# Optimization experiments

Measured on AMD Instinct MI355X. Metric: run time of the kernel, lower is better.

The kernel has to match this reference:

```python
import jax, jax.numpy as jnp
import numpy as np

H = 64
NG = 100000   # gene nodes
ND = 30000    # disease nodes
NE = 1500000  # gda edges (gene -> disease)
NL = 500000   # supervision (label) edges


def setup_inputs() -> dict:
    key = jax.random.key(0)
    ks = jax.random.split(key, 20)
    s = 0.1
    inp = {
        "gene_emb":    jax.random.normal(ks[0], (NG, H), jnp.float32) * s,
        "disease_emb": jax.random.normal(ks[1], (ND, H), jnp.float32) * s,
    }
    wnames = ["w1_gd_l", "w1_gd_r", "w1_dg_l", "w1_dg_r",
              "w2_gd_l", "w2_gd_r", "w2_dg_l", "w2_dg_r"]
    for i, n in enumerate(wnames):
        inp[n] = jax.random.normal(ks[2 + i], (H, H), jnp.float32) * s
    for i, n in enumerate(["b1_gd", "b1_dg", "b2_gd", "b2_dg"]):
        inp[n] = jax.random.normal(ks[10 + i], (H,), jnp.float32) * 0.01
    inp["edge_src"]  = jax.random.randint(ks[14], (NE,), 0, NG)
    inp["edge_dst"]  = jax.random.randint(ks[15], (NE,), 0, ND)
    inp["label_src"] = jax.random.randint(ks[16], (NL,), 0, NG)
    inp["label_dst"] = jax.random.randint(ks[17], (NL,), 0, ND)
    return inp


def _sage(x_src, x_dst, src, dst, n_dst, wl, wr, b):
    # SAGEConv (mean aggr): lin_l(mean_{j in N(i)} x_j) + lin_r(x_i) + b
    msum = jax.ops.segment_sum(x_src[src], dst, num_segments=n_dst)
    cnt = jax.ops.segment_sum(jnp.ones((src.shape[0], 1), x_src.dtype), dst,
                              num_segments=n_dst)
    mean = msum / jnp.maximum(cnt, 1.0)
    return mean @ wl + x_dst @ wr + b


def reference(gene_emb, disease_emb,
              w1_gd_l, w1_gd_r, b1_gd, w1_dg_l, w1_dg_r, b1_dg,
              w2_gd_l, w2_gd_r, b2_gd, w2_dg_l, w2_dg_r, b2_dg,
              edge_src, edge_dst, label_src, label_dst):
    # layer 1 (hetero: gene->disease via gda, disease->gene via rev_gda)
    h_d = jax.nn.relu(_sage(gene_emb, disease_emb, edge_src, edge_dst, ND,
                            w1_gd_l, w1_gd_r, b1_gd))
    h_g = jax.nn.relu(_sage(disease_emb, gene_emb, edge_dst, edge_src, NG,
                            w1_dg_l, w1_dg_r, b1_dg))
    # layer 2 (no activation)
    h_d2 = _sage(h_g, h_d, edge_src, edge_dst, ND, w2_gd_l, w2_gd_r, b2_gd)
    h_g2 = _sage(h_d, h_g, edge_dst, edge_src, NG, w2_dg_l, w2_dg_r, b2_dg)
    # classifier: dot product over label edges
    return jnp.sum(h_g2[label_src] * h_d2[label_dst], axis=-1)
```

## Files before the change

### kernel.cpp

```cpp
#include <hip/hip_runtime.h>
#include <hip/hip_bf16.h>

#define H 64
#define SCAN_CHUNK 512
#define NB1 512

typedef unsigned short u16;
typedef unsigned int u32;
typedef __attribute__((ext_vector_type(8))) __bf16 bf16x8;
typedef __attribute__((ext_vector_type(4))) float f32x4;

__device__ __forceinline__ float bflo(u32 u) {
    return __builtin_bit_cast(float, u << 16);
}
__device__ __forceinline__ float bfhi(u32 u) {
    return __builtin_bit_cast(float, u & 0xffff0000u);
}
__device__ __forceinline__ u16 bf16rne(float f) {
    u32 u = __builtin_bit_cast(u32, f);
    return (u16)((u + 0x7FFFu + ((u >> 16) & 1u)) >> 16);
}

__global__ __launch_bounds__(256) void fused_count_convert_kernel(
    const int* __restrict__ es, const int* __restrict__ ed,
    int* __restrict__ histD, int* __restrict__ histG,
    int ne, int shiftD, int shiftG,
    const float* __restrict__ a, u16* __restrict__ oa, long long na4,
    const float* __restrict__ b, u16* __restrict__ ob, long long nb4)
{
    if (blockIdx.x < NB1) {
        __shared__ int lhd[256], lhg[256];
        const int tid = threadIdx.x;
        lhd[tid] = 0; lhg[tid] = 0;
        __syncthreads();
        const int chunk = (ne + NB1 - 1) / NB1;
        const int e0 = blockIdx.x * chunk;
        const int e1 = min(e0 + chunk, ne);
        for (int e = e0 + tid; e < e1; e += 256) {
            atomicAdd(&lhd[ed[e] >> shiftD], 1);
            atomicAdd(&lhg[es[e] >> shiftG], 1);
        }
        __syncthreads();
        histD[tid * NB1 + blockIdx.x] = lhd[tid];
        histG[tid * NB1 + blockIdx.x] = lhg[tid];
        return;
    }
    long long i = (long long)(blockIdx.x - NB1) * 256 + threadIdx.x;
    const float* src; u16* dst; long long q;
    if (i < na4) { src = a; dst = oa; q = i; }
    else if (i < na4 + nb4) { src = b; dst = ob; q = i - na4; }
    else return;
    float4 v = *(const float4*)&src[q * 4];
    ushort4 o;
    o.x = bf16rne(v.x); o.y = bf16rne(v.y);
    o.z = bf16rne(v.z); o.w = bf16rne(v.w);
    *(ushort4*)&dst[q * 4] = o;
}

__global__ __launch_bounds__(256) void scan_reduce_kernel(
    const int* __restrict__ a1, int n1, const int* __restrict__ a2, int n2,
    int B1, int* __restrict__ partial)
{
    const int b = blockIdx.x;
    const int* a; int n, base;
    if (b < B1) { a = a1; n = n1; base = b * SCAN_CHUNK; }
    else        { a = a2; n = n2; base = (b - B1) * SCAN_CHUNK; }
    int t = threadIdx.x;
    int i0 = base + 2 * t, i1 = i0 + 1;
    int v = ((i0 < n) ? a[i0] : 0) + ((i1 < n) ? a[i1] : 0);
    #pragma unroll
    for (int off = 32; off > 0; off >>= 1) v += __shfl_down(v, off, 64);
    __shared__ int ws[4];
    if ((t & 63) == 0) ws[t >> 6] = v;
    __syncthreads();
    if (t == 0) partial[b] = ws[0] + ws[1] + ws[2] + ws[3];
}

__global__ __launch_bounds__(256) void scan_apply_kernel(
    const int* __restrict__ a1, int* __restrict__ out1, int n1,
    const int* __restrict__ a2, int* __restrict__ out2, int n2,
    int B1, int nbtot, const int* __restrict__ partial)
{
    __shared__ int sExcl[1024];
    __shared__ int ws[4];
    const int tid = threadIdx.x;
    const int lane = tid & 63, wid = tid >> 6;

    int j0 = 4 * tid;
    int p0 = (j0 + 0 < nbtot) ? partial[j0 + 0] : 0;
    int p1 = (j0 + 1 < nbtot) ? partial[j0 + 1] : 0;
    int p2 = (j0 + 2 < nbtot) ? partial[j0 + 2] : 0;
    int p3 = (j0 + 3 < nbtot) ? partial[j0 + 3] : 0;
    int psum = p0 + p1 + p2 + p3;
    int P = psum;
    #pragma unroll
    for (int off = 1; off < 64; off <<= 1) {
        int u = __shfl_up(P, off, 64);
        if (lane >= off) P += u;
    }
    if (lane == 63) ws[wid] = P;
    __syncthreads();
    int wbase = 0;
    #pragma unroll
    for (int w = 0; w < 4; ++w) wbase += (w < wid) ? ws[w] : 0;
    int e = wbase + (P - psum);
    sExcl[j0 + 0] = e;
    sExcl[j0 + 1] = e + p0;
    sExcl[j0 + 2] = e + p0 + p1;
    sExcl[j0 + 3] = e + p0 + p1 + p2;
    __syncthreads();

    const int b = blockIdx.x;
    int tot1 = sExcl[B1 - 1] + ((B1 - 1 < nbtot) ? partial[B1 - 1] : 0);
    int myOff = sExcl[b] - ((b >= B1) ? tot1 : 0);
    if (b == 0 && tid == 0) {
        int tot2 = sExcl[nbtot - 1] + partial[nbtot - 1] - tot1;
        out1[n1] = tot1;
        out2[n2] = tot2;
    }
    __syncthreads();

    const int* a; int* out; int n, base;
    if (b < B1) { a = a1; out = out1; n = n1; base = b * SCAN_CHUNK; }
    else        { a = a2; out = out2; n = n2; base = (b - B1) * SCAN_CHUNK; }
    int i0 = base + 2 * tid, i1 = i0 + 1;
    int x0 = (i0 < n) ? a[i0] : 0;
    int x1 = (i1 < n) ? a[i1] : 0;
    int p = x0 + x1;
    int Q = p;
    #pragma unroll
    for (int off = 1; off < 64; off <<= 1) {
        int u = __shfl_up(Q, off, 64);
        if (lane >= off) Q += u;
    }
    if (lane == 63) ws[wid] = Q;
    __syncthreads();
    int waveBase = 0;
    #pragma unroll
    for (int w = 0; w < 4; ++w) waveBase += (w < wid) ? ws[w] : 0;
    int off0 = myOff + waveBase + (Q - p);
    if (i0 < n) out[i0] = off0;
    if (i1 < n) out[i1] = off0 + x0;
}

__global__ __launch_bounds__(256) void part_scatter_kernel(
    const int* __restrict__ es, const int* __restrict__ ed,
    const int* __restrict__ baseD, const int* __restrict__ baseG,
    u32* __restrict__ pairD, u32* __restrict__ pairG,
    int ne, int shiftD, int shiftG)
{
    __shared__ int curD[256], curG[256];
    const int tid = threadIdx.x;
    curD[tid] = baseD[tid * NB1 + blockIdx.x];
    curG[tid] = baseG[tid * NB1 + blockIdx.x];
    __syncthreads();
    const int maskD = (1 << shiftD) - 1;
    const int maskG = (1 << shiftG) - 1;
    const int chunk = (ne + NB1 - 1) / NB1;
    const int e0 = blockIdx.x * chunk;
    const int e1 = min(e0 + chunk, ne);
    for (int e = e0 + tid; e < e1; e += 256) {
        int s = es[e], d = ed[e];
        int pD = atomicAdd(&curD[d >> shiftD], 1);
        pairD[pD] = ((u32)(d & maskD) << 17) | (u32)s;
        int pG = atomicAdd(&curG[s >> shiftG], 1);
        pairG[pG] = ((u32)(s & maskG) << 17) | (u32)d;
    }
}

__global__ __launch_bounds__(256) void csr_build_kernel(
    const u32* __restrict__ pairD, const int* __restrict__ baseD,
    int* __restrict__ rowD, int* __restrict__ idxD, int nd, int shiftD, int nbktD,
    const u32* __restrict__ pairG, const int* __restrict__ baseG,
    int* __restrict__ rowG, int* __restrict__ idxG, int ng, int shiftG, int nbktG)
{
    __shared__ int lcnt[512], lcur[512];
    __shared__ int ws[4];
    const int j = blockIdx.x & 255;
    const int isG = blockIdx.x >> 8;
    const u32* pair; const int* base; int* row; int* idx; int n, shift, nbkt;
    if (isG) { pair = pairG; base = baseG; row = rowG; idx = idxG; n = ng; shift = shiftG; nbkt = nbktG; }
    else     { pair = pairD; base = baseD; row = rowD; idx = idxD; n = nd; shift = shiftD; nbkt = nbktD; }
    if (j >= nbkt) return;

    const int tid = threadIdx.x;
    const int nLo = j << shift;
    const int nHi = min(nLo + (1 << shift), n);
    const int range = nHi - nLo;
    const int segBase = base[j * NB1];
    const int segEnd  = base[(j + 1) * NB1];

    lcnt[tid] = 0; lcnt[tid + 256] = 0;
    __syncthreads();
    for (int t = segBase + tid; t < segEnd; t += 256)
        atomicAdd(&lcnt[pair[t] >> 17], 1);
    __syncthreads();

    int i0 = 2 * tid, i1 = i0 + 1;
    int c0 = (i0 < range) ? lcnt[i0] : 0;
    int c1 = (i1 < range) ? lcnt[i1] : 0;
    int p = c0 + c1;
    int P = p;
    const int lane = tid & 63, wid = tid >> 6;
    #pragma unroll
    for (int off = 1; off < 64; off <<= 1) {
        int u = __shfl_up(P, off, 64);
        if (lane >= off) P += u;
    }
    if (lane == 63) ws[wid] = P;
    __syncthreads();
    int waveBase = 0;
    #pragma unroll
    for (int w = 0; w < 4; ++w) waveBase += (w < wid) ? ws[w] : 0;
    int o0 = segBase + waveBase + (P - p);
    int o1 = o0 + c0;
    if (i0 < range) { row[nLo + i0] = o0; lcur[i0] = o0; }
    if (i1 < range) { row[nLo + i1] = o1; lcur[i1] = o1; }
    if (nHi == n && tid == 0) row[n] = segEnd;
    __syncthreads();

    for (int t = segBase + tid; t < segEnd; t += 256) {
        u32 pr = pair[t];
        int pos = atomicAdd(&lcur[pr >> 17], 1);
        idx[pos] = (int)(pr & 0x1FFFFu);
    }
}

__global__ __launch_bounds__(256) void gather_mean_kernel(
    const u16* __restrict__ srcD, const u16* __restrict__ srcG,
    const int* __restrict__ rowD, const int* __restrict__ idxD,
    const int* __restrict__ rowG, const int* __restrict__ idxG,
    u16* __restrict__ outD, u16* __restrict__ outG, int nd, int ng)
{
    int hw = blockIdx.x * 8 + (threadIdx.x >> 5);
    int l5 = threadIdx.x & 31;
    const u16* src; const int* row; const int* idx; u16* out; int node;
    if (hw < nd)            { src = srcD; row = rowD; idx = idxD; out = outD; node = hw; }
    else if (hw < nd + ng)  { src = srcG; row = rowG; idx = idxG; out = outG; node = hw - nd; }
    else return;

    const int sub = l5 >> 3;
    const int c8 = l5 & 7;
    int beg = row[node], end = row[node + 1];

    float a0[8], a1[8], a2[8], a3[8];
    #pragma unroll
    for (int j = 0; j < 8; ++j) { a0[j] = 0.f; a1[j] = 0.f; a2[j] = 0.f; a3[j] = 0.f; }

    int i = beg;
    for (; i + 16 <= end; i += 16) {
        int s0 = idx[i + sub];
        int s1 = idx[i + 4 + sub];
        int s2 = idx[i + 8 + sub];
        int s3 = idx[i + 12 + sub];
        uint4 v0 = *((const uint4*)(src + (size_t)s0 * H) + c8);
        uint4 v1 = *((const uint4*)(src + (size_t)s1 * H) + c8);
        uint4 v2 = *((const uint4*)(src + (size_t)s2 * H) + c8);
        uint4 v3 = *((const uint4*)(src + (size_t)s3 * H) + c8);
        a0[0] += bflo(v0.x); a0[1] += bfhi(v0.x); a0[2] += bflo(v0.y); a0[3] += bfhi(v0.y);
        a0[4] += bflo(v0.z); a0[5] += bfhi(v0.z); a0[6] += bflo(v0.w); a0[7] += bfhi(v0.w);
        a1[0] += bflo(v1.x); a1[1] += bfhi(v1.x); a1[2] += bflo(v1.y); a1[3] += bfhi(v1.y);
        a1[4] += bflo(v1.z); a1[5] += bfhi(v1.z); a1[6] += bflo(v1.w); a1[7] += bfhi(v1.w);
        a2[0] += bflo(v2.x); a2[1] += bfhi(v2.x); a2[2] += bflo(v2.y); a2[3] += bfhi(v2.y);
        a2[4] += bflo(v2.z); a2[5] += bfhi(v2.z); a2[6] += bflo(v2.w); a2[7] += bfhi(v2.w);
        a3[0] += bflo(v3.x); a3[1] += bfhi(v3.x); a3[2] += bflo(v3.y); a3[3] += bfhi(v3.y);
        a3[4] += bflo(v3.z); a3[5] += bfhi(v3.z); a3[6] += bflo(v3.w); a3[7] += bfhi(v3.w);
    }
    if (i + 8 <= end) {
        int s0 = idx[i + sub];
        int s1 = idx[i + 4 + sub];
        uint4 v0 = *((const uint4*)(src + (size_t)s0 * H) + c8);
        uint4 v1 = *((const uint4*)(src + (size_t)s1 * H) + c8);
        a0[0] += bflo(v0.x); a0[1] += bfhi(v0.x); a0[2] += bflo(v0.y); a0[3] += bfhi(v0.y);
        a0[4] += bflo(v0.z); a0[5] += bfhi(v0.z); a0[6] += bflo(v0.w); a0[7] += bfhi(v0.w);
        a1[0] += bflo(v1.x); a1[1] += bfhi(v1.x); a1[2] += bflo(v1.y); a1[3] += bfhi(v1.y);
        a1[4] += bflo(v1.z); a1[5] += bfhi(v1.z); a1[6] += bflo(v1.w); a1[7] += bfhi(v1.w);
        i += 8;
    }
    if (i + 4 <= end) {
        int s0 = idx[i + sub];
        uint4 v0 = *((const uint4*)(src + (size_t)s0 * H) + c8);
        a2[0] += bflo(v0.x); a2[1] += bfhi(v0.x); a2[2] += bflo(v0.y); a2[3] += bfhi(v0.y);
        a2[4] += bflo(v0.z); a2[5] += bfhi(v0.z); a2[6] += bflo(v0.w); a2[7] += bfhi(v0.w);
        i += 4;
    }
    if (i + sub < end) {
        int s1 = idx[i + sub];
        uint4 v1 = *((const uint4*)(src + (size_t)s1 * H) + c8);
        a3[0] += bflo(v1.x); a3[1] += bfhi(v1.x); a3[2] += bflo(v1.y); a3[3] += bfhi(v1.y);
        a3[4] += bflo(v1.z); a3[5] += bfhi(v1.z); a3[6] += bflo(v1.w); a3[7] += bfhi(v1.w);
    }
    float acc[8];
    #pragma unroll
    for (int j = 0; j < 8; ++j) acc[j] = (a0[j] + a1[j]) + (a2[j] + a3[j]);
    #pragma unroll
    for (int j = 0; j < 8; ++j) {
        acc[j] += __shfl_xor(acc[j], 8, 64);
        acc[j] += __shfl_xor(acc[j], 16, 64);
    }
    if (sub == 0) {
        float inv = 1.0f / fmaxf((float)(end - beg), 1.0f);
        u32 w0 = (u32)bf16rne(acc[0] * inv) | ((u32)bf16rne(acc[1] * inv) << 16);
        u32 w1 = (u32)bf16rne(acc[2] * inv) | ((u32)bf16rne(acc[3] * inv) << 16);
        u32 w2 = (u32)bf16rne(acc[4] * inv) | ((u32)bf16rne(acc[5] * inv) << 16);
        u32 w3 = (u32)bf16rne(acc[6] * inv) | ((u32)bf16rne(acc[7] * inv) << 16);
        uint4 pk = make_uint4(w0, w1, w2, w3);
        *(uint4*)(out + (size_t)node * H + c8 * 8) = pk;
    }
}

template <bool RELU>
__global__ __launch_bounds__(256) void sage_mm_mfma_kernel(
    const u16* __restrict__ meanD, const u16* __restrict__ xD, u16* __restrict__ outD,
    const float* __restrict__ wlD, const float* __restrict__ wrD,
    const float* __restrict__ bD, int nd,
    const u16* __restrict__ meanG, const u16* __restrict__ xG, u16* __restrict__ outG,
    const float* __restrict__ wlG, const float* __restrict__ wrG,
    const float* __restrict__ bG, int ng, int MBD)
{
    __shared__ u16 sB[16 * 64 * 8];
    int b = blockIdx.x;
    const u16 *mean, *x; u16* out; const float *wl, *wr, *bias; int n;
    if (b < MBD) { mean = meanD; x = xD; out = outD; wl = wlD; wr = wrD; bias = bD; n = nd; }
    else { b -= MBD; mean = meanG; x = xG; out = outG; wl = wlG; wr = wrG; bias = bG; n = ng; }

    const int tid = threadIdx.x;
    for (int i = tid; i < 4096; i += 256) {
        int k = i >> 6, ncol = i & 63;
        int q = (k >> 3) & 3, j = k & 7, t = ncol >> 4, n15 = ncol & 15;
        int lane = q * 16 + n15;
        int c0 = k >> 5;
        sB[(((c0 + 0) * 4 + t) * 64 + lane) * 8 + j] = bf16rne(wl[i]);
        sB[(((c0 + 2) * 4 + t) * 64 + lane) * 8 + j] = bf16rne(wr[i]);
    }
    __syncthreads();

    const int lane = tid & 63;
    const int wave = tid >> 6;
    const int m = lane & 15;
    const int q = lane >> 4;

    bf16x8 Bf[16];
    {
        const uint4* sB4 = (const uint4*)sB;
        #pragma unroll
        for (int f = 0; f < 16; ++f)
            Bf[f] = __builtin_bit_cast(bf16x8, sB4[f * 64 + lane]);
    }
    float bv[4];
    #pragma unroll
    for (int t = 0; t < 4; ++t) bv[t] = bias[t * 16 + m];

    const int row0 = b * 256;
    #pragma unroll
    for (int r = 0; r < 4; ++r) {
        int rbase = row0 + (wave + 4 * r) * 16;
        if (rbase >= n) break;
        int gr = min(rbase + m, n - 1);
        const uint4* mrow = (const uint4*)(mean + (size_t)gr * H);
        const uint4* xrow = (const uint4*)(x + (size_t)gr * H);
        bf16x8 A0 = __builtin_bit_cast(bf16x8, mrow[q]);
        bf16x8 A1 = __builtin_bit_cast(bf16x8, mrow[q + 4]);
        bf16x8 A2 = __builtin_bit_cast(bf16x8, xrow[q]);
        bf16x8 A3 = __builtin_bit_cast(bf16x8, xrow[q + 4]);
        f32x4 acc[4];
        #pragma unroll
        for (int t = 0; t < 4; ++t) acc[t] = (f32x4){bv[t], bv[t], bv[t], bv[t]};
        #pragma unroll
        for (int t = 0; t < 4; ++t) {
            acc[t] = __builtin_amdgcn_mfma_f32_16x16x32_bf16(A0, Bf[0 * 4 + t], acc[t], 0, 0, 0);
            acc[t] = __builtin_amdgcn_mfma_f32_16x16x32_bf16(A1, Bf[1 * 4 + t], acc[t], 0, 0, 0);
            acc[t] = __builtin_amdgcn_mfma_f32_16x16x32_bf16(A2, Bf[2 * 4 + t], acc[t], 0, 0, 0);
            acc[t] = __builtin_amdgcn_mfma_f32_16x16x32_bf16(A3, Bf[3 * 4 + t], acc[t], 0, 0, 0);
        }
        #pragma unroll
        for (int reg = 0; reg < 4; ++reg) {
            int orow = rbase + q * 4 + reg;
            if (orow < n) {
                u16* op = out + (size_t)orow * H;
                #pragma unroll
                for (int t = 0; t < 4; ++t) {
                    float v = acc[t][reg];
                    if (RELU) v = fmaxf(v, 0.0f);
                    op[t * 16 + m] = bf16rne(v);
                }
            }
        }
    }
}

__global__ __launch_bounds__(256) void classify_kernel(
    const u16* __restrict__ hg2, const u16* __restrict__ hd2,
    const int* __restrict__ ls, const int* __restrict__ ld,
    float* __restrict__ out, int nl)
{
    long long t = (long long)blockIdx.x * blockDim.x + threadIdx.x;
    int e = (int)(t >> 3);
    int c8 = (int)(t & 7);
    if (e >= nl) return;
    int a = ls[e];
    int b = ld[e];
    uint4 ua = *((const uint4*)(hg2 + (size_t)a * H) + c8);
    uint4 ub = *((const uint4*)(hd2 + (size_t)b * H) + c8);
    float v = bflo(ua.x) * bflo(ub.x) + bfhi(ua.x) * bfhi(ub.x)
            + bflo(ua.y) * bflo(ub.y) + bfhi(ua.y) * bfhi(ub.y)
            + bflo(ua.z) * bflo(ub.z) + bfhi(ua.z) * bfhi(ub.z)
            + bflo(ua.w) * bflo(ub.w) + bfhi(ua.w) * bfhi(ub.w);
    v += __shfl_xor(v, 1, 64);
    v += __shfl_xor(v, 2, 64);
    v += __shfl_xor(v, 4, 64);
    if (c8 == 0) out[e] = v;
}

extern "C" void kernel_launch(void* const* d_in, const int* in_sizes, int n_in,
                              void* d_out, int out_size, void* d_ws, size_t ws_size,
                              hipStream_t stream)
{
    const float* gene  = (const float*)d_in[0];
    const float* dis   = (const float*)d_in[1];
    const float* w1gdl = (const float*)d_in[2];
    const float* w1gdr = (const float*)d_in[3];
    const float* w1dgl = (const float*)d_in[4];
    const float* w1dgr = (const float*)d_in[5];
    const float* w2gdl = (const float*)d_in[6];
    const float* w2gdr = (const float*)d_in[7];
    const float* w2dgl = (const float*)d_in[8];
    const float* w2dgr = (const float*)d_in[9];
    const float* b1gd  = (const float*)d_in[10];
    const float* b1dg  = (const float*)d_in[11];
    const float* b2gd  = (const float*)d_in[12];
    const float* b2dg  = (const float*)d_in[13];
    const int* es = (const int*)d_in[14];
    const int* ed = (const int*)d_in[15];
    const int* ls = (const int*)d_in[16];
    const int* ld = (const int*)d_in[17];

    const int ng = in_sizes[0] / H;
    const int nd = in_sizes[1] / H;
    const int ne = in_sizes[14];
    const int nl = in_sizes[16];

    int shiftD = 0; while (((nd + (1 << shiftD) - 1) >> shiftD) > 256) ++shiftD;
    int shiftG = 0; while (((ng + (1 << shiftG) - 1) >> shiftG) > 256) ++shiftG;
    const int nbktD = (nd + (1 << shiftD) - 1) >> shiftD;
    const int nbktG = (ng + (1 << shiftG) - 1) >> shiftG;
    const int n1 = 256 * NB1;

    int* rowD = (int*)d_ws;
    int* rowG = rowD + nd + 1;
    int* idxD = rowG + ng + 1;
    int* idxG = idxD + ne;
    u16* geneBf = (u16*)(idxG + ne);
    u16* disBf  = geneBf + (size_t)ng * H;
    u16* h1Dbf  = disBf + (size_t)nd * H;
    u16* h1Gbf  = h1Dbf + (size_t)nd * H;
    u16* h2Dbf  = h1Gbf + (size_t)ng * H;
    u16* h2Gbf  = h2Dbf + (size_t)nd * H;
    uintptr_t p = (uintptr_t)(h2Gbf + (size_t)ng * H);
    p = (p + 15) & ~(uintptr_t)15;
    u16* MD = (u16*)p;
    u16* MG = MD + (size_t)nd * H;
    int* histD = (int*)p;
    int* histG = histD + n1;
    int* baseD = histG + n1;
    int* baseG = baseD + n1 + 1;
    int* partial  = baseG + n1 + 1;
    uintptr_t pp = (uintptr_t)(partial + 1024);
    pp = (pp + 15) & ~(uintptr_t)15;
    u32* pairD = (u32*)pp;
    u32* pairG = pairD + ne;

    const long long na4 = (long long)ng * H / 4;
    const long long nb4 = (long long)nd * H / 4;
    const int convBlocks = (int)((na4 + nb4 + 255) / 256);
    fused_count_convert_kernel<<<NB1 + convBlocks, 256, 0, stream>>>(
        es, ed, histD, histG, ne, shiftD, shiftG,
        gene, geneBf, na4, dis, disBf, nb4);

    const int B1 = n1 / SCAN_CHUNK;
    const int nbtot = 2 * B1;
    scan_reduce_kernel<<<nbtot, 256, 0, stream>>>(histD, n1, histG, n1, B1, partial);
    scan_apply_kernel<<<nbtot, 256, 0, stream>>>(histD, baseD, n1,
                                                 histG, baseG, n1, B1, nbtot, partial);

    part_scatter_kernel<<<NB1, 256, 0, stream>>>(es, ed, baseD, baseG,
                                                 pairD, pairG, ne, shiftD, shiftG);
    csr_build_kernel<<<512, 256, 0, stream>>>(
        pairD, baseD, rowD, idxD, nd, shiftD, nbktD,
        pairG, baseG, rowG, idxG, ng, shiftG, nbktG);

    const int gatherBlocks = (nd + ng + 7) / 8;
    const int MBD = (nd + 255) / 256;
    const int MBG = (ng + 255) / 256;

    gather_mean_kernel<<<gatherBlocks, 256, 0, stream>>>(
        geneBf, disBf, rowD, idxD, rowG, idxG, MD, MG, nd, ng);
    sage_mm_mfma_kernel<true><<<MBD + MBG, 256, 0, stream>>>(
        MD, disBf, h1Dbf, w1gdl, w1gdr, b1gd, nd,
        MG, geneBf, h1Gbf, w1dgl, w1dgr, b1dg, ng, MBD);

    gather_mean_kernel<<<gatherBlocks, 256, 0, stream>>>(
        h1Gbf, h1Dbf, rowD, idxD, rowG, idxG, MD, MG, nd, ng);
    sage_mm_mfma_kernel<false><<<MBD + MBG, 256, 0, stream>>>(
        MD, h1Dbf, h2Dbf, w2gdl, w2gdr, b2gd, nd,
        MG, h1Gbf, h2Gbf, w2dgl, w2dgr, b2dg, ng, MBD);

    {
        long long threads = (long long)nl * 8;
        int blocks = (int)((threads + 255) / 256);
        classify_kernel<<<blocks, 256, 0, stream>>>(h2Gbf, h2Dbf, ls, ld,
                                                    (float*)d_out, nl);
    }
}
```

Before: 376.8 us.

## Gather layer-1 gene features from a scaled FP8 copy instead of BF16

The convert kernel now also writes an FP8 (scaled by 16) copy of gene embeddings. The first-layer disease-side gather reads these 8-bit rows, which halves the bytes fetched per edge, and undoes the scale in the mean. The gather loop unroll also drops from 16 to 8 edges per iteration with two accumulator sets instead of four. In exchange there is extra conversion work and write traffic up front, and the lower precision may hurt accuracy.

Result: faster. 349.8 us (-7.2%).

```diff
diff --git a/kernel.cpp b/kernel.cpp
--- a/kernel.cpp
+++ b/kernel.cpp
@@ -7,8 +7,10 @@
 
 typedef unsigned short u16;
 typedef unsigned int u32;
+typedef unsigned char u8;
 typedef __attribute__((ext_vector_type(8))) __bf16 bf16x8;
 typedef __attribute__((ext_vector_type(4))) float f32x4;
+typedef __attribute__((ext_vector_type(2))) float f32x2;
 
 __device__ __forceinline__ float bflo(u32 u) {
     return __builtin_bit_cast(float, u << 16);
@@ -25,7 +27,8 @@
     const int* __restrict__ es, const int* __restrict__ ed,
     int* __restrict__ histD, int* __restrict__ histG,
     int ne, int shiftD, int shiftG,
-    const float* __restrict__ a, u16* __restrict__ oa, long long na4,
+    const float* __restrict__ a, u16* __restrict__ oa, u32* __restrict__ oa8,
+    long long na4,
     const float* __restrict__ b, u16* __restrict__ ob, long long nb4)
 {
     if (blockIdx.x < NB1) {
@@ -46,15 +49,24 @@
         return;
     }
     long long i = (long long)(blockIdx.x - NB1) * 256 + threadIdx.x;
-    const float* src; u16* dst; long long q;
-    if (i < na4) { src = a; dst = oa; q = i; }
-    else if (i < na4 + nb4) { src = b; dst = ob; q = i - na4; }
-    else return;
-    float4 v = *(const float4*)&src[q * 4];
-    ushort4 o;
-    o.x = bf16rne(v.x); o.y = bf16rne(v.y);
-    o.z = bf16rne(v.z); o.w = bf16rne(v.w);
-    *(ushort4*)&dst[q * 4] = o;
+    if (i < na4) {
+        float4 v = *(const float4*)&a[i * 4];
+        ushort4 o;
+        o.x = bf16rne(v.x); o.y = bf16rne(v.y);
+        o.z = bf16rne(v.z); o.w = bf16rne(v.w);
+        *(ushort4*)&oa[i * 4] = o;
+        int r = 0;
+        r = __builtin_amdgcn_cvt_pk_fp8_f32(v.x * 16.0f, v.y * 16.0f, r, false);
+        r = __builtin_amdgcn_cvt_pk_fp8_f32(v.z * 16.0f, v.w * 16.0f, r, true);
+        oa8[i] = (u32)r;
+    } else if (i < na4 + nb4) {
+        long long q = i - na4;
+        float4 v = *(const float4*)&b[q * 4];
+        ushort4 o;
+        o.x = bf16rne(v.x); o.y = bf16rne(v.y);
+        o.z = bf16rne(v.z); o.w = bf16rne(v.w);
+        *(ushort4*)&ob[q * 4] = o;
+    }
 }
 
 __global__ __launch_bounds__(256) void scan_reduce_kernel(
@@ -111,7 +123,7 @@
     __syncthreads();
 
     const int b = blockIdx.x;
-    int tot1 = sExcl[B1 - 1] + ((B1 - 1 < nbtot) ? partial[B1 - 1] : 0);
+    int tot1 = sExcl[B1 - 1] + partial[B1 - 1];
     int myOff = sExcl[b] - ((b >= B1) ? tot1 : 0);
     if (b == 0 && tid == 0) {
         int tot2 = sExcl[nbtot - 1] + partial[nbtot - 1] - tot1;
@@ -226,73 +238,96 @@
     }
 }
 
+template <bool F8D>
 __global__ __launch_bounds__(256) void gather_mean_kernel(
-    const u16* __restrict__ srcD, const u16* __restrict__ srcG,
+    const void* __restrict__ srcD_, const u16* __restrict__ srcG,
     const int* __restrict__ rowD, const int* __restrict__ idxD,
     const int* __restrict__ rowG, const int* __restrict__ idxG,
     u16* __restrict__ outD, u16* __restrict__ outG, int nd, int ng)
 {
     int hw = blockIdx.x * 8 + (threadIdx.x >> 5);
     int l5 = threadIdx.x & 31;
-    const u16* src; const int* row; const int* idx; u16* out; int node;
-    if (hw < nd)            { src = srcD; row = rowD; idx = idxD; out = outD; node = hw; }
-    else if (hw < nd + ng)  { src = srcG; row = rowG; idx = idxG; out = outG; node = hw - nd; }
-    else return;
-
+    if (hw >= nd + ng) return;
+    const bool isD = hw < nd;
     const int sub = l5 >> 3;
     const int c8 = l5 & 7;
+    const int* row; const int* idx; u16* out; int node;
+    if (isD) { row = rowD; idx = idxD; out = outD; node = hw; }
+    else     { row = rowG; idx = idxG; out = outG; node = hw - nd; }
     int beg = row[node], end = row[node + 1];
 
-    float a0[8], a1[8], a2[8], a3[8];
-    #pragma unroll
-    for (int j = 0; j < 8; ++j) { a0[j] = 0.f; a1[j] = 0.f; a2[j] = 0.f; a3[j] = 0.f; }
-
-    int i = beg;
-    for (; i + 16 <= end; i += 16) {
-        int s0 = idx[i + sub];
-        int s1 = idx[i + 4 + sub];
-        int s2 = idx[i + 8 + sub];
-        int s3 = idx[i + 12 + sub];
-        uint4 v0 = *((const uint4*)(src + (size_t)s0 * H) + c8);
-        uint4 v1 = *((const uint4*)(src + (size_t)s1 * H) + c8);
-        uint4 v2 = *((const uint4*)(src + (size_t)s2 * H) + c8);
-        uint4 v3 = *((const uint4*)(src + (size_t)s3 * H) + c8);
-        a0[0] += bflo(v0.x); a0[1] += bfhi(v0.x); a0[2] += bflo(v0.y); a0[3] += bfhi(v0.y);
-        a0[4] += bflo(v0.z); a0[5] += bfhi(v0.z); a0[6] += bflo(v0.w); a0[7] += bfhi(v0.w);
-        a1[0] += bflo(v1.x); a1[1] += bfhi(v1.x); a1[2] += bflo(v1.y); a1[3] += bfhi(v1.y);
-        a1[4] += bflo(v1.z); a1[5] += bfhi(v1.z); a1[6] += bflo(v1.w); a1[7] += bfhi(v1.w);
-        a2[0] += bflo(v2.x); a2[1] += bfhi(v2.x); a2[2] += bflo(v2.y); a2[3] += bfhi(v2.y);
-        a2[4] += bflo(v2.z); a2[5] += bfhi(v2.z); a2[6] += bflo(v2.w); a2[7] += bfhi(v2.w);
-        a3[0] += bflo(v3.x); a3[1] += bfhi(v3.x); a3[2] += bflo(v3.y); a3[3] += bfhi(v3.y);
-        a3[4] += bflo(v3.z); a3[5] += bfhi(v3.z); a3[6] += bflo(v3.w); a3[7] += bfhi(v3.w);
-    }
-    if (i + 8 <= end) {
-        int s0 = idx[i + sub];
-        int s1 = idx[i + 4 + sub];
-        uint4 v0 = *((const uint4*)(src + (size_t)s0 * H) + c8);
-        uint4 v1 = *((const uint4*)(src + (size_t)s1 * H) + c8);
-        a0[0] += bflo(v0.x); a0[1] += bfhi(v0.x); a0[2] += bflo(v0.y); a0[3] += bfhi(v0.y);
-        a0[4] += bflo(v0.z); a0[5] += bfhi(v0.z); a0[6] += bflo(v0.w); a0[7] += bfhi(v0.w);
-        a1[0] += bflo(v1.x); a1[1] += bfhi(v1.x); a1[2] += bflo(v1.y); a1[3] += bfhi(v1.y);
-        a1[4] += bflo(v1.z); a1[5] += bfhi(v1.z); a1[6] += bflo(v1.w); a1[7] += bfhi(v1.w);
-        i += 8;
-    }
-    if (i + 4 <= end) {
-        int s0 = idx[i + sub];
-        uint4 v0 = *((const uint4*)(src + (size_t)s0 * H) + c8);
-        a2[0] += bflo(v0.x); a2[1] += bfhi(v0.x); a2[2] += bflo(v0.y); a2[3] += bfhi(v0.y);
-        a2[4] += bflo(v0.z); a2[5] += bfhi(v0.z); a2[6] += bflo(v0.w); a2[7] += bfhi(v0.w);
-        i += 4;
-    }
-    if (i + sub < end) {
-        int s1 = idx[i + sub];
-        uint4 v1 = *((const uint4*)(src + (size_t)s1 * H) + c8);
-        a3[0] += bflo(v1.x); a3[1] += bfhi(v1.x); a3[2] += bflo(v1.y); a3[3] += bfhi(v1.y);
-        a3[4] += bflo(v1.z); a3[5] += bfhi(v1.z); a3[6] += bflo(v1.w); a3[7] += bfhi(v1.w);
-    }
+    float a0[8], a1[8];
+    #pragma unroll
+    for (int j = 0; j < 8; ++j) { a0[j] = 0.f; a1[j] = 0.f; }
+
+    if (F8D && isD) {
+        const u8* src8 = (const u8*)srcD_;
+        int i = beg;
+        for (; i + 8 <= end; i += 8) {
+            int s0 = idx[i + sub];
+            int s1 = idx[i + 4 + sub];
+            uint2 v0 = *((const uint2*)(src8 + (size_t)s0 * 64) + c8);
+            uint2 v1 = *((const uint2*)(src8 + (size_t)s1 * 64) + c8);
+            f32x2 f;
+            f = __builtin_amdgcn_cvt_pk_f32_fp8((int)v0.x, false); a0[0] += f.x; a0[1] += f.y;
+            f = __builtin_amdgcn_cvt_pk_f32_fp8((int)v0.x, true);  a0[2] += f.x; a0[3] += f.y;
+            f = __builtin_amdgcn_cvt_pk_f32_fp8((int)v0.y, false); a0[4] += f.x; a0[5] += f.y;
+            f = __builtin_amdgcn_cvt_pk_f32_fp8((int)v0.y, true);  a0[6] += f.x; a0[7] += f.y;
+            f = __builtin_amdgcn_cvt_pk_f32_fp8((int)v1.x, false); a1[0] += f.x; a1[1] += f.y;
+            f = __builtin_amdgcn_cvt_pk_f32_fp8((int)v1.x, true);  a1[2] += f.x; a1[3] += f.y;
+            f = __builtin_amdgcn_cvt_pk_f32_fp8((int)v1.y, false); a1[4] += f.x; a1[5] += f.y;
+            f = __builtin_amdgcn_cvt_pk_f32_fp8((int)v1.y, true);  a1[6] += f.x; a1[7] += f.y;
+        }
+        if (i + 4 <= end) {
+            int s0 = idx[i + sub];
+            uint2 v0 = *((const uint2*)(src8 + (size_t)s0 * 64) + c8);
+            f32x2 f;
+            f = __builtin_amdgcn_cvt_pk_f32_fp8((int)v0.x, false); a0[0] += f.x; a0[1] += f.y;
+            f = __builtin_amdgcn_cvt_pk_f32_fp8((int)v0.x, true);  a0[2] += f.x; a0[3] += f.y;
+            f = __builtin_amdgcn_cvt_pk_f32_fp8((int)v0.y, false); a0[4] += f.x; a0[5] += f.y;
+            f = __builtin_amdgcn_cvt_pk_f32_fp8((int)v0.y, true);  a0[6] += f.x; a0[7] += f.y;
+            i += 4;
+        }
+        if (i + sub < end) {
+            int s1 = idx[i + sub];
+            uint2 v1 = *((const uint2*)(src8 + (size_t)s1 * 64) + c8);
+            f32x2 f;
+            f = __builtin_amdgcn_cvt_pk_f32_fp8((int)v1.x, false); a1[0] += f.x; a1[1] += f.y;
+            f = __builtin_amdgcn_cvt_pk_f32_fp8((int)v1.x, true);  a1[2] += f.x; a1[3] += f.y;
+            f = __builtin_amdgcn_cvt_pk_f32_fp8((int)v1.y, false); a1[4] += f.x; a1[5] += f.y;
+            f = __builtin_amdgcn_cvt_pk_f32_fp8((int)v1.y, true);  a1[6] += f.x; a1[7] += f.y;
+        }
+    } else {
+        const u16* src = isD ? (const u16*)srcD_ : srcG;
+        int i = beg;
+        for (; i + 8 <= end; i += 8) {
+            int s0 = idx[i + sub];
+            int s1 = idx[i + 4 + sub];
+            uint4 v0 = *((const uint4*)(src + (size_t)s0 * H) + c8);
+            uint4 v1 = *((const uint4*)(src + (size_t)s1 * H) + c8);
+            a0[0] += bflo(v0.x); a0[1] += bfhi(v0.x); a0[2] += bflo(v0.y); a0[3] += bfhi(v0.y);
+            a0[4] += bflo(v0.z); a0[5] += bfhi(v0.z); a0[6] += bflo(v0.w); a0[7] += bfhi(v0.w);
+            a1[0] += bflo(v1.x); a1[1] += bfhi(v1.x); a1[2] += bflo(v1.y); a1[3] += bfhi(v1.y);
+            a1[4] += bflo(v1.z); a1[5] += bfhi(v1.z); a1[6] += bflo(v1.w); a1[7] += bfhi(v1.w);
+        }
+        if (i + 4 <= end) {
+            int s0 = idx[i + sub];
+            uint4 v0 = *((const uint4*)(src + (size_t)s0 * H) + c8);
+            a0[0] += bflo(v0.x); a0[1] += bfhi(v0.x); a0[2] += bflo(v0.y); a0[3] += bfhi(v0.y);
+            a0[4] += bflo(v0.z); a0[5] += bfhi(v0.z); a0[6] += bflo(v0.w); a0[7] += bfhi(v0.w);
+            i += 4;
+        }
+        if (i + sub < end) {
+            int s1 = idx[i + sub];
+            uint4 v1 = *((const uint4*)(src + (size_t)s1 * H) + c8);
+            a1[0] += bflo(v1.x); a1[1] += bfhi(v1.x); a1[2] += bflo(v1.y); a1[3] += bfhi(v1.y);
+            a1[4] += bflo(v1.z); a1[5] += bfhi(v1.z); a1[6] += bflo(v1.w); a1[7] += bfhi(v1.w);
+        }
+    }
+
     float acc[8];
     #pragma unroll
-    for (int j = 0; j < 8; ++j) acc[j] = (a0[j] + a1[j]) + (a2[j] + a3[j]);
+    for (int j = 0; j < 8; ++j) acc[j] = a0[j] + a1[j];
     #pragma unroll
     for (int j = 0; j < 8; ++j) {
         acc[j] += __shfl_xor(acc[j], 8, 64);
@@ -300,6 +335,7 @@
     }
     if (sub == 0) {
         float inv = 1.0f / fmaxf((float)(end - beg), 1.0f);
+        if (F8D && isD) inv *= 0.0625f;
         u32 w0 = (u32)bf16rne(acc[0] * inv) | ((u32)bf16rne(acc[1] * inv) << 16);
         u32 w1 = (u32)bf16rne(acc[2] * inv) | ((u32)bf16rne(acc[3] * inv) << 16);
         u32 w2 = (u32)bf16rne(acc[4] * inv) | ((u32)bf16rne(acc[5] * inv) << 16);
@@ -456,7 +492,10 @@
     u16* h1Gbf  = h1Dbf + (size_t)nd * H;
     u16* h2Dbf  = h1Gbf + (size_t)ng * H;
     u16* h2Gbf  = h2Dbf + (size_t)nd * H;
-    uintptr_t p = (uintptr_t)(h2Gbf + (size_t)ng * H);
+    uintptr_t pf8 = (uintptr_t)(h2Gbf + (size_t)ng * H);
+    pf8 = (pf8 + 15) & ~(uintptr_t)15;
+    u32* geneF8 = (u32*)pf8;
+    uintptr_t p = (uintptr_t)(geneF8 + (size_t)ng * 16);
     p = (p + 15) & ~(uintptr_t)15;
     u16* MD = (u16*)p;
     u16* MG = MD + (size_t)nd * H;
@@ -475,7 +514,7 @@
     const int convBlocks = (int)((na4 + nb4 + 255) / 256);
     fused_count_convert_kernel<<<NB1 + convBlocks, 256, 0, stream>>>(
         es, ed, histD, histG, ne, shiftD, shiftG,
-        gene, geneBf, na4, dis, disBf, nb4);
+        gene, geneBf, geneF8, na4, dis, disBf, nb4);
 
     const int B1 = n1 / SCAN_CHUNK;
     const int nbtot = 2 * B1;
@@ -493,13 +532,13 @@
     const int MBD = (nd + 255) / 256;
     const int MBG = (ng + 255) / 256;
 
-    gather_mean_kernel<<<gatherBlocks, 256, 0, stream>>>(
-        geneBf, disBf, rowD, idxD, rowG, idxG, MD, MG, nd, ng);
+    gather_mean_kernel<true><<<gatherBlocks, 256, 0, stream>>>(
+        geneF8, disBf, rowD, idxD, rowG, idxG, MD, MG, nd, ng);
     sage_mm_mfma_kernel<true><<<MBD + MBG, 256, 0, stream>>>(
         MD, disBf, h1Dbf, w1gdl, w1gdr, b1gd, nd,
         MG, geneBf, h1Gbf, w1dgl, w1dgr, b1dg, ng, MBD);
 
-    gather_mean_kernel<<<gatherBlocks, 256, 0, stream>>>(
+    gather_mean_kernel<false><<<gatherBlocks, 256, 0, stream>>>(
         h1Gbf, h1Dbf, rowD, idxD, rowG, idxG, MD, MG, nd, ng);
     sage_mm_mfma_kernel<false><<<MBD + MBG, 256, 0, stream>>>(
         MD, h1Dbf, h2Dbf, w2gdl, w2gdr, b2gd, nd,
```
